# Optimization experiments

Hardware: AMD Instinct MI355X
Metric: run time of the kernel (lower is better)

Reference implementation:

```python
import jax, jax.numpy as jnp
import numpy as np

K = 24          # num_eigh
D_MODEL = 768   # d_in == d_out
STATE = 100     # LDS state_dim
BSZ = 1
SEQ = 2048


def setup_inputs() -> dict:
    key = jax.random.key(0)
    ks = jax.random.split(key, 8)
    x = jax.random.normal(ks[0], (BSZ, SEQ, D_MODEL), dtype=jnp.float32)
    input_pos = jnp.arange(SEQ, dtype=jnp.int32)
    M_inputs = jax.random.normal(ks[1], (D_MODEL, D_MODEL), dtype=jnp.float32) * 0.02
    M_filters = jax.random.normal(ks[2], (K, D_MODEL), dtype=jnp.float32) * 0.02
    # LDS params: diagonal A (stable, |a|<1), B maps scalar input -> state,
    # C maps state -> 2K outputs, Dv is scalar-input feedthrough to 2K outputs.
    A = jax.random.uniform(ks[3], (STATE,), dtype=jnp.float32, minval=0.0, maxval=0.99)
    Bm = jax.random.normal(ks[4], (STATE,), dtype=jnp.float32) * 0.1
    C = jax.random.normal(ks[5], (STATE, 2 * K), dtype=jnp.float32) * 0.1
    Dv = jax.random.normal(ks[6], (2 * K,), dtype=jnp.float32) * 0.1
    return {"x": x, "input_pos": input_pos, "M_inputs": M_inputs,
            "M_filters": M_filters, "A": A, "Bm": Bm, "C": C, "Dv": Dv}


def reference(x, input_pos, M_inputs, M_filters, A, Bm, C, Dv):
    bsz, seq_len, d_in = x.shape
    k = M_filters.shape[0]
    # input projection (use_approx branch)
    xp = x @ M_inputs                                   # (b, s, d)
    # flatten per-channel scalar sequences: (b*d, s)
    u = xp.transpose(0, 2, 1).reshape(bsz * d_in, seq_len)
    ut = u.T                                            # (s, N) for scan over time
    h0 = jnp.zeros((bsz * d_in, A.shape[0]), dtype=xp.dtype)

    def step(h, u_t):
        # h: (N, state), u_t: (N,) scalar input per lane
        h = h * A[None, :] + u_t[:, None] * Bm[None, :]
        y = h @ C + u_t[:, None] * Dv[None, :]          # (N, 2K)
        return h, y

    _, ys = jax.lax.scan(step, h0, ut)                  # (s, N, 2K)
    # U: (b, s, 2K, d)
    U = ys.transpose(1, 0, 2).reshape(bsz, d_in, seq_len, 2 * k).transpose(0, 2, 3, 1)
    spectral_plus = jnp.einsum('bskd,kd->bsd', U[:, :, k:, :], M_filters)
    spectral_minus = jnp.einsum('bskd,kd->bsd', U[:, :, :k, :], M_filters)
    return spectral_plus + spectral_minus
```

## Files before the change

### kernel.cpp

```cpp
#include <hip/hip_runtime.h>

#define SEQ   2048
#define DM    768
#define ST    100
#define KF    24
#define NC    32
#define KJ    128
#define NJ    112

using half8   = __attribute__((ext_vector_type(8))) _Float16;
using float4v = __attribute__((ext_vector_type(4))) float;
using ush8    = __attribute__((ext_vector_type(8))) short;

__device__ __forceinline__ unsigned short f2h(float v) {
    union { _Float16 h; unsigned short u; } cv;
    cv.h = (_Float16)v;
    return cv.u;
}
__device__ __forceinline__ void async16(const void* g, void* l) {
    __builtin_amdgcn_global_load_lds(
        (const __attribute__((address_space(1))) unsigned int*)g,
        (__attribute__((address_space(3))) unsigned int*)l, 16, 0, 0);
}

__global__ __launch_bounds__(256) void prep(const float* __restrict__ x,
                                            const float* __restrict__ Mi,
                                            const float* __restrict__ C,
                                            const float* __restrict__ Dv,
                                            const float* __restrict__ Mf,
                                            const float* __restrict__ Av,
                                            const float* __restrict__ Bv,
                                            unsigned short* __restrict__ Mh,
                                            unsigned short* __restrict__ Xh,
                                            float* __restrict__ WpT,
                                            float* __restrict__ evec,
                                            float* __restrict__ Apow,
                                            unsigned short* __restrict__ Eh,
                                            unsigned short* __restrict__ Qh) {
    __shared__ float tl[64][65];
    int bid = blockIdx.x, t = threadIdx.x;
    if (bid < 144) {
        int i0 = (bid / 12) * 64, d0 = (bid % 12) * 64;
        int tx = t & 63, ty = t >> 6;
#pragma unroll
        for (int r = ty; r < 64; r += 4)
            tl[r][tx] = Mi[(i0 + r) * DM + d0 + tx];
        __syncthreads();
#pragma unroll
        for (int r = ty; r < 64; r += 4)
            Mh[(size_t)(d0 + r) * DM + i0 + tx] = f2h(tl[tx][r]);
    } else if (bid < 912) {
        int idx8 = (bid - 144) * 256 + t;
        int s = idx8 / (DM / 8), i0 = (idx8 % (DM / 8)) * 8;
        const float* xp = x + (size_t)s * DM + i0;
        float4 v0 = *(const float4*)xp;
        float4 v1 = *(const float4*)(xp + 4);
        float av[8] = {v0.x, v0.y, v0.z, v0.w, v1.x, v1.y, v1.z, v1.w};
        ush8 hh;
#pragma unroll
        for (int q = 0; q < 8; ++q) hh[q] = (short)f2h(av[q]);
        *(ush8*)(Xh + (size_t)s * DM + i0) = hh;
    } else if (bid < 1212) {
        int tid = (bid - 912) * 256 + t;
        if (tid < ST * DM) {
            int d = tid / ST, j = tid % ST;
            float s = 0.f;
#pragma unroll
            for (int k = 0; k < KF; ++k)
                s += (C[j * 2 * KF + k] + C[j * 2 * KF + KF + k]) * Mf[k * DM + d];
            WpT[tid] = s;
        }
        if (tid < DM) {
            float s = 0.f;
#pragma unroll
            for (int k = 0; k < KF; ++k)
                s += (Dv[k] + Dv[KF + k]) * Mf[k * DM + tid];
            evec[tid] = s;
        }
    } else {
        if (t < KJ) {
            bool ja = (t < ST);
            float a = ja ? Av[t] : 0.f;
            float b = ja ? Bv[t] : 0.f;
            float p = 1.f;
            for (int dlt = 0; dlt < 64; ++dlt) {
                if (ja) Apow[dlt * ST + t] = p;
                if (t < NJ) Qh[t * 64 + 63 - dlt] = f2h(b * p);
                p *= a;
                Eh[dlt * KJ + t] = f2h(p);
            }
            if (ja) Apow[64 * ST + t] = p;
        }
    }
}

__global__ __launch_bounds__(256) void gemm_mfma(const unsigned short* __restrict__ Mh,
                                                 const unsigned short* __restrict__ Xh,
                                                 float* __restrict__ ut) {
    __shared__ unsigned short As[64 * 64];
    __shared__ unsigned short Bs[64 * 64];
    int t = threadIdx.x;
    int tile = blockIdx.x;
    int d0 = (tile % (DM / 64)) * 64;
    int s0 = (tile / (DM / 64)) * 64;
    int wave = t >> 6, lane = t & 63;
    int m16 = lane & 15, quad = lane >> 4;
    int r0 = t >> 3,         q0 = ((t & 7) - r0) & 7;
    int r1 = (t + 256) >> 3, q1 = (((t + 256) & 7) - r1) & 7;
    float4v acc[4];
#pragma unroll
    for (int nt = 0; nt < 4; ++nt) acc[nt] = (float4v){0.f, 0.f, 0.f, 0.f};
    for (int k0 = 0; k0 < DM; k0 += 64) {
        __syncthreads();
        async16(&Mh[(size_t)(d0 + r0) * DM + k0 + q0 * 8], &As[(size_t)t * 8]);
        async16(&Xh[(size_t)(s0 + r0) * DM + k0 + q0 * 8], &Bs[(size_t)t * 8]);
        async16(&Mh[(size_t)(d0 + r1) * DM + k0 + q1 * 8], &As[(size_t)(t + 256) * 8]);
        async16(&Xh[(size_t)(s0 + r1) * DM + k0 + q1 * 8], &Bs[(size_t)(t + 256) * 8]);
        __syncthreads();
        int arow = wave * 16 + m16;
        half8 af[2], bf[4][2];
#pragma unroll
        for (int h = 0; h < 2; ++h)
            af[h] = *(half8*)&As[arow * 64 + (((h * 4 + quad) + arow) & 7) * 8];
#pragma unroll
        for (int nt = 0; nt < 4; ++nt) {
            int brow = nt * 16 + m16;
#pragma unroll
            for (int h = 0; h < 2; ++h)
                bf[nt][h] = *(half8*)&Bs[brow * 64 + (((h * 4 + quad) + brow) & 7) * 8];
        }
#pragma unroll
        for (int h = 0; h < 2; ++h)
#pragma unroll
            for (int nt = 0; nt < 4; ++nt)
                acc[nt] = __builtin_amdgcn_mfma_f32_16x16x32_f16(af[h], bf[nt][h], acc[nt], 0, 0, 0);
    }
#pragma unroll
    for (int nt = 0; nt < 4; ++nt) {
        int dd = d0 + wave * 16 + quad * 4;
        int ss = s0 + nt * 16 + m16;
#pragma unroll
        for (int i = 0; i < 4; ++i)
            ut[(size_t)(dd + i) * SEQ + ss] = acc[nt][i];
    }
}

__global__ __launch_bounds__(256) void scanf_k(float* ut,
                                               const unsigned short* __restrict__ Qh,
                                               const float* __restrict__ WpT,
                                               const float* __restrict__ Apow,
                                               const float* __restrict__ Bv,
                                               const float* __restrict__ evec,
                                               unsigned short* __restrict__ Gh) {
    __shared__ float hl[64][120];
    __shared__ float kk[128];
    int t = threadIdx.x;
    int m0 = blockIdx.x * 64;
    int d0 = blockIdx.x * 2;
    if (t < 128) {
        int dlt = t & 63, dloc = t >> 6;
        const float* wrow = WpT + (d0 + dloc) * ST;
        float s = 0.f;
        for (int j = 0; j < ST; ++j)
            s = fmaf(Bv[j] * Apow[dlt * ST + j], wrow[j], s);
        kk[t] = s;
    }
    int wave = t >> 6, lane = t & 63;
    int m16 = lane & 15, quad = lane >> 4;
    {
        float4v acc[7];
#pragma unroll
        for (int nt = 0; nt < 7; ++nt) acc[nt] = (float4v){0.f, 0.f, 0.f, 0.f};
#pragma unroll
        for (int ks = 0; ks < 2; ++ks) {
            size_t ao = (size_t)(m0 + wave * 16 + m16) * 64 + ks * 32 + quad * 8;
            float4 a0 = *(const float4*)(ut + ao);
            float4 a1 = *(const float4*)(ut + ao + 4);
            float av[8] = {a0.x, a0.y, a0.z, a0.w, a1.x, a1.y, a1.z, a1.w};
            half8 ah;
#pragma unroll
            for (int q = 0; q < 8; ++q) ah[q] = (_Float16)av[q];
#pragma unroll
            for (int nt = 0; nt < 7; ++nt) {
                half8 bh = *(const half8*)(Qh + (nt * 16 + m16) * 64 + ks * 32 + quad * 8);
                acc[nt] = __builtin_amdgcn_mfma_f32_16x16x32_f16(ah, bh, acc[nt], 0, 0, 0);
            }
        }
#pragma unroll
        for (int nt = 0; nt < 7; ++nt)
#pragma unroll
            for (int i = 0; i < 4; ++i)
                hl[wave * 16 + quad * 4 + i][nt * 16 + m16] = acc[nt][i];
    }
    __syncthreads();
    {
        int j = t & 127, dloc = t >> 7;
        int d = d0 + dloc;
        bool ja = (j < ST);
        float a64 = ja ? Apow[64 * ST + j] : 0.f;
        float w   = ja ? WpT[d * ST + j] : 0.f;
        float hs = 0.f;
        for (int c = 0; c < NC; ++c) {
            Gh[((size_t)c * DM + d) * KJ + j] = f2h(w * hs);
            float add = ja ? hl[dloc * 32 + c][j] : 0.f;
            hs = fmaf(a64, hs, add);
        }
    }
    if (t < 64) {
        int dloc = t >> 5, c = t & 31;
        int d = d0 + dloc;
        size_t off = (size_t)d * SEQ + c * 64;
        float uu[64];
#pragma unroll
        for (int q = 0; q < 16; ++q) {
            float4 v = *(const float4*)(ut + off + q * 4);
            uu[q * 4 + 0] = v.x; uu[q * 4 + 1] = v.y;
            uu[q * 4 + 2] = v.z; uu[q * 4 + 3] = v.w;
        }
        float e = evec[d];
        float y[64];
#pragma unroll
        for (int tt = 0; tt < 64; ++tt) y[tt] = e * uu[tt];
        const float* kt = &kk[dloc * 64];
#pragma unroll
        for (int dlt = 0; dlt < 64; ++dlt) {
            float k = kt[dlt];
#pragma unroll
            for (int tt = dlt; tt < 64; ++tt)
                y[tt] = fmaf(k, uu[tt - dlt], y[tt]);
        }
#pragma unroll
        for (int q = 0; q < 16; ++q) {
            float4 v = make_float4(y[q * 4 + 0], y[q * 4 + 1], y[q * 4 + 2], y[q * 4 + 3]);
            *(float4*)(ut + off + q * 4) = v;
        }
    }
}

__global__ __launch_bounds__(256) void inter(const unsigned short* __restrict__ Eh,
                                             const unsigned short* __restrict__ Gh,
                                             const float* __restrict__ yintra,
                                             float* __restrict__ out) {
    __shared__ float yl[64][68];
    int c = blockIdx.x;
    int d0 = blockIdx.y * 64;
    int t = threadIdx.x;
#pragma unroll
    for (int it = 0; it < 4; ++it) {
        int idx = t + it * 256;
        int row = idx >> 4, col4 = (idx & 15) * 4;
        float4 v = *(const float4*)&yintra[(size_t)(d0 + row) * SEQ + c * 64 + col4];
        yl[col4 + 0][row] = v.x;
        yl[col4 + 1][row] = v.y;
        yl[col4 + 2][row] = v.z;
        yl[col4 + 3][row] = v.w;
    }
    __syncthreads();
    int wave = t >> 6, lane = t & 63;
    int wn = wave * 16;
    int m16 = lane & 15, quad = lane >> 4;
    float4v acc[4];
#pragma unroll
    for (int mt = 0; mt < 4; ++mt) acc[mt] = (float4v){0.f, 0.f, 0.f, 0.f};
#pragma unroll
    for (int ks = 0; ks < 4; ++ks) {
        half8 bh = *(const half8*)(Gh + ((size_t)c * DM + d0 + wn + m16) * KJ + ks * 32 + quad * 8);
#pragma unroll
        for (int mt = 0; mt < 4; ++mt) {
            half8 ah = *(const half8*)(Eh + (mt * 16 + m16) * KJ + ks * 32 + quad * 8);
            acc[mt] = __builtin_amdgcn_mfma_f32_16x16x32_f16(ah, bh, acc[mt], 0, 0, 0);
        }
    }
#pragma unroll
    for (int mt = 0; mt < 4; ++mt) {
        int tt = mt * 16 + quad * 4;
        int dcol = wn + m16;
#pragma unroll
        for (int i = 0; i < 4; ++i) {
            float v = acc[mt][i] + yl[tt + i][dcol];
            out[(size_t)(c * 64 + tt + i) * DM + d0 + dcol] = v;
        }
    }
}

extern "C" void kernel_launch(void* const* d_in, const int* in_sizes, int n_in,
                              void* d_out, int out_size, void* d_ws, size_t ws_size,
                              hipStream_t stream) {
    const float* x  = (const float*)d_in[0];
    const float* Mi = (const float*)d_in[2];
    const float* Mf = (const float*)d_in[3];
    const float* Av = (const float*)d_in[4];
    const float* Bv = (const float*)d_in[5];
    const float* C  = (const float*)d_in[6];
    const float* Dv = (const float*)d_in[7];
    float* out = (float*)d_out;

    float* ut   = (float*)d_ws;
    float* WpT  = ut + (size_t)DM * SEQ;
    float* ev   = WpT + DM * ST;
    float* Apow = ev + DM;
    unsigned short* Mh = (unsigned short*)(Apow + 65 * ST);
    unsigned short* Xh = Mh + (size_t)DM * DM;
    unsigned short* Eh = Xh + (size_t)SEQ * DM;
    unsigned short* Qh = Eh + 64 * KJ;
    unsigned short* Gh = Qh + NJ * 64;

    prep<<<1213, 256, 0, stream>>>(x, Mi, C, Dv, Mf, Av, Bv, Mh, Xh,
                                   WpT, ev, Apow, Eh, Qh);
    gemm_mfma<<<(DM / 64) * (SEQ / 64), 256, 0, stream>>>(Mh, Xh, ut);
    scanf_k<<<384, 256, 0, stream>>>(ut, Qh, WpT, Apow, Bv, ev, Gh);
    inter<<<dim3(NC, DM / 64), 256, 0, stream>>>(Eh, Gh, ut, out);
}
```

Baseline: 113.6 us.

## Double-buffer GEMM tiles and spread intra-chunk convolution across all waves

The input-projection GEMM now double-buffers its LDS tiles, issuing the async loads for the next k-slice before computing on the current one, so one barrier per iteration replaces two. In the scan kernel, the causal 64-tap intra-chunk convolution previously ran on only 64 threads with 64-element register arrays. It is now split across all 256 threads, each computing a balanced pair of 8-output blocks (low and high), reading inputs staged in a new padded LDS buffer. The inter kernel's transpose buffer padding also changes from 68 to 65. The cost is extra LDS use, and the balanced split relies on careful index arithmetic.

```diff
diff --git a/kernel.cpp b/kernel.cpp
--- a/kernel.cpp
+++ b/kernel.cpp
@@ -97,8 +97,8 @@
 __global__ __launch_bounds__(256) void gemm_mfma(const unsigned short* __restrict__ Mh,
                                                  const unsigned short* __restrict__ Xh,
                                                  float* __restrict__ ut) {
-    __shared__ unsigned short As[64 * 64];
-    __shared__ unsigned short Bs[64 * 64];
+    __shared__ unsigned short As[2][64 * 64];
+    __shared__ unsigned short Bs[2][64 * 64];
     int t = threadIdx.x;
     int tile = blockIdx.x;
     int d0 = (tile % (DM / 64)) * 64;
@@ -110,31 +110,39 @@
     float4v acc[4];
 #pragma unroll
     for (int nt = 0; nt < 4; ++nt) acc[nt] = (float4v){0.f, 0.f, 0.f, 0.f};
+
+#define STAGE(buf, kk0)                                                                     \
+    async16(&Mh[(size_t)(d0 + r0) * DM + (kk0) + q0 * 8], &As[buf][(size_t)t * 8]);         \
+    async16(&Xh[(size_t)(s0 + r0) * DM + (kk0) + q0 * 8], &Bs[buf][(size_t)t * 8]);         \
+    async16(&Mh[(size_t)(d0 + r1) * DM + (kk0) + q1 * 8], &As[buf][(size_t)(t + 256) * 8]); \
+    async16(&Xh[(size_t)(s0 + r1) * DM + (kk0) + q1 * 8], &Bs[buf][(size_t)(t + 256) * 8]);
+
+    STAGE(0, 0);
+    __syncthreads();
+    int cur = 0;
+    int arow = wave * 16 + m16;
     for (int k0 = 0; k0 < DM; k0 += 64) {
-        __syncthreads();
-        async16(&Mh[(size_t)(d0 + r0) * DM + k0 + q0 * 8], &As[(size_t)t * 8]);
-        async16(&Xh[(size_t)(s0 + r0) * DM + k0 + q0 * 8], &Bs[(size_t)t * 8]);
-        async16(&Mh[(size_t)(d0 + r1) * DM + k0 + q1 * 8], &As[(size_t)(t + 256) * 8]);
-        async16(&Xh[(size_t)(s0 + r1) * DM + k0 + q1 * 8], &Bs[(size_t)(t + 256) * 8]);
-        __syncthreads();
-        int arow = wave * 16 + m16;
+        if (k0 + 64 < DM) { STAGE(cur ^ 1, k0 + 64); }
         half8 af[2], bf[4][2];
 #pragma unroll
         for (int h = 0; h < 2; ++h)
-            af[h] = *(half8*)&As[arow * 64 + (((h * 4 + quad) + arow) & 7) * 8];
+            af[h] = *(half8*)&As[cur][arow * 64 + (((h * 4 + quad) + arow) & 7) * 8];
 #pragma unroll
         for (int nt = 0; nt < 4; ++nt) {
             int brow = nt * 16 + m16;
 #pragma unroll
             for (int h = 0; h < 2; ++h)
-                bf[nt][h] = *(half8*)&Bs[brow * 64 + (((h * 4 + quad) + brow) & 7) * 8];
+                bf[nt][h] = *(half8*)&Bs[cur][brow * 64 + (((h * 4 + quad) + brow) & 7) * 8];
         }
 #pragma unroll
         for (int h = 0; h < 2; ++h)
 #pragma unroll
             for (int nt = 0; nt < 4; ++nt)
                 acc[nt] = __builtin_amdgcn_mfma_f32_16x16x32_f16(af[h], bf[nt][h], acc[nt], 0, 0, 0);
-    }
+        __syncthreads();
+        cur ^= 1;
+    }
+#undef STAGE
 #pragma unroll
     for (int nt = 0; nt < 4; ++nt) {
         int dd = d0 + wave * 16 + quad * 4;
@@ -154,6 +162,7 @@
                                                unsigned short* __restrict__ Gh) {
     __shared__ float hl[64][120];
     __shared__ float kk[128];
+    __shared__ float ul[2][32][65];
     int t = threadIdx.x;
     int m0 = blockIdx.x * 64;
     int d0 = blockIdx.x * 2;
@@ -168,14 +177,17 @@
     int wave = t >> 6, lane = t & 63;
     int m16 = lane & 15, quad = lane >> 4;
     {
+        int r = wave * 16 + m16;
         float4v acc[7];
 #pragma unroll
         for (int nt = 0; nt < 7; ++nt) acc[nt] = (float4v){0.f, 0.f, 0.f, 0.f};
 #pragma unroll
         for (int ks = 0; ks < 2; ++ks) {
-            size_t ao = (size_t)(m0 + wave * 16 + m16) * 64 + ks * 32 + quad * 8;
+            size_t ao = (size_t)(m0 + r) * 64 + ks * 32 + quad * 8;
             float4 a0 = *(const float4*)(ut + ao);
             float4 a1 = *(const float4*)(ut + ao + 4);
+            *(float4*)&ul[r >> 5][r & 31][ks * 32 + quad * 8]     = a0;
+            *(float4*)&ul[r >> 5][r & 31][ks * 32 + quad * 8 + 4] = a1;
             float av[8] = {a0.x, a0.y, a0.z, a0.w, a1.x, a1.y, a1.z, a1.w};
             half8 ah;
 #pragma unroll
@@ -206,34 +218,57 @@
             hs = fmaf(a64, hs, add);
         }
     }
-    if (t < 64) {
-        int dloc = t >> 5, c = t & 31;
+    {
+        int q = wave;
+        int p = t & 63;
+        int dloc = p >> 5, c = p & 31;
         int d = d0 + dloc;
+        int lo0 = q * 8, hi0 = (7 - q) * 8;
+        const float* kt = &kk[dloc * 64];
+        const float* us = &ul[dloc][c][0];
+        float e = evec[d];
+        float ylo[8], yhi[8];
+#pragma unroll
+        for (int z = 0; z < 8; ++z) {
+            ylo[z] = e * us[lo0 + z];
+            yhi[z] = e * us[hi0 + z];
+        }
+        for (int i = 0; i < lo0; ++i) {
+            float u = us[i];
+#pragma unroll
+            for (int z = 0; z < 8; ++z) {
+                ylo[z] = fmaf(kt[lo0 + z - i], u, ylo[z]);
+                yhi[z] = fmaf(kt[hi0 + z - i], u, yhi[z]);
+            }
+        }
+#pragma unroll
+        for (int zi = 0; zi < 8; ++zi) {
+            float u = us[lo0 + zi];
+#pragma unroll
+            for (int z = zi; z < 8; ++z)
+                ylo[z] = fmaf(kt[z - zi], u, ylo[z]);
+#pragma unroll
+            for (int z = 0; z < 8; ++z)
+                yhi[z] = fmaf(kt[hi0 - lo0 + z - zi], u, yhi[z]);
+        }
+        for (int i = lo0 + 8; i < hi0; ++i) {
+            float u = us[i];
+#pragma unroll
+            for (int z = 0; z < 8; ++z)
+                yhi[z] = fmaf(kt[hi0 + z - i], u, yhi[z]);
+        }
+#pragma unroll
+        for (int zi = 0; zi < 8; ++zi) {
+            float u = us[hi0 + zi];
+#pragma unroll
+            for (int z = zi; z < 8; ++z)
+                yhi[z] = fmaf(kt[z - zi], u, yhi[z]);
+        }
         size_t off = (size_t)d * SEQ + c * 64;
-        float uu[64];
-#pragma unroll
-        for (int q = 0; q < 16; ++q) {
-            float4 v = *(const float4*)(ut + off + q * 4);
-            uu[q * 4 + 0] = v.x; uu[q * 4 + 1] = v.y;
-            uu[q * 4 + 2] = v.z; uu[q * 4 + 3] = v.w;
-        }
-        float e = evec[d];
-        float y[64];
-#pragma unroll
-        for (int tt = 0; tt < 64; ++tt) y[tt] = e * uu[tt];
-        const float* kt = &kk[dloc * 64];
-#pragma unroll
-        for (int dlt = 0; dlt < 64; ++dlt) {
-            float k = kt[dlt];
-#pragma unroll
-            for (int tt = dlt; tt < 64; ++tt)
-                y[tt] = fmaf(k, uu[tt - dlt], y[tt]);
-        }
-#pragma unroll
-        for (int q = 0; q < 16; ++q) {
-            float4 v = make_float4(y[q * 4 + 0], y[q * 4 + 1], y[q * 4 + 2], y[q * 4 + 3]);
-            *(float4*)(ut + off + q * 4) = v;
-        }
+        *(float4*)(ut + off + lo0)     = make_float4(ylo[0], ylo[1], ylo[2], ylo[3]);
+        *(float4*)(ut + off + lo0 + 4) = make_float4(ylo[4], ylo[5], ylo[6], ylo[7]);
+        *(float4*)(ut + off + hi0)     = make_float4(yhi[0], yhi[1], yhi[2], yhi[3]);
+        *(float4*)(ut + off + hi0 + 4) = make_float4(yhi[4], yhi[5], yhi[6], yhi[7]);
     }
 }
 
@@ -241,7 +276,7 @@
                                              const unsigned short* __restrict__ Gh,
                                              const float* __restrict__ yintra,
                                              float* __restrict__ out) {
-    __shared__ float yl[64][68];
+    __shared__ float yl[64][65];
     int c = blockIdx.x;
     int d0 = blockIdx.y * 64;
     int t = threadIdx.x;
```

Measured after the change: 117.7 us. 3.6% more time.
